# Optimization experiments

Hardware: AMD Instinct MI355X
Metric: run time of the kernel (lower is better)

## Reference

```python
import jax, jax.numpy as jnp
import numpy as np
from jax import lax

USER_NUM = 60000
ITEM_NUM = 40000
N_NODES = USER_NUM + ITEM_NUM
EMB = 64
NNZ = 3200000
N_LAYERS = 3
ALPHA = 0.1


def setup_inputs() -> dict:
    key = jax.random.key(0)
    k1, k2, k3, k4, k5 = jax.random.split(key, 5)
    rows = jax.random.randint(k1, (NNZ,), 0, N_NODES, dtype=jnp.int32)
    cols = jax.random.randint(k2, (NNZ,), 0, N_NODES, dtype=jnp.int32)
    # normalized adjacency values are small positives
    vals = jax.random.uniform(k3, (NNZ,), dtype=jnp.float32) * 0.05
    user_emb = jax.random.normal(k4, (USER_NUM, EMB), dtype=jnp.float32) * 0.1
    item_emb = jax.random.normal(k5, (ITEM_NUM, EMB), dtype=jnp.float32) * 0.1
    return {"rows": rows, "cols": cols, "vals": vals,
            "user_emb": user_emb, "item_emb": item_emb}


def reference(rows, cols, vals, user_emb, item_emb):
    # ego = cat(user, item); e_out starts at zeros (first forward call).
    ego = jnp.concatenate([user_emb, item_emb], axis=0)  # [N, d]
    e0 = jnp.zeros_like(ego)

    def step(e, _):
        # torch.sparse.mm(A, e.clone().detach()) -> SpMM with stop_gradient,
        # matching the original's detach of the propagated state.
        gathered = vals[:, None] * lax.stop_gradient(e)[cols]  # [nnz, d]
        msg = jax.ops.segment_sum(gathered, rows, num_segments=N_NODES)
        e_new = (1.0 - ALPHA) * msg + ego
        return e_new, None

    e_out, _ = lax.scan(step, e0, None, length=N_LAYERS)
    return e_out[:USER_NUM], e_out[USER_NUM:]
```

## Files before the change

### kernel.cpp

```cpp
#include <hip/hip_runtime.h>
#include <hip/hip_fp16.h>


#define USER_NUM 60000
#define ITEM_NUM 40000
#define N_NODES  100000
#define EMB      64
#define NNZ      3200000
#define OMA      0.9f
#define BR       128
#define NB       782
#define TILE     4096
#define CAP      4608

typedef float f32x4 __attribute__((ext_vector_type(4)));

__global__ __launch_bounds__(256) void ego_to_half(const float* __restrict__ ue,
                                                   const float* __restrict__ ie,
                                                   __half* __restrict__ dst) {
    int t = blockIdx.x * 256 + threadIdx.x;
    const int total8 = N_NODES * EMB / 8;
    if (t >= total8) return;
    size_t f0 = (size_t)t * 8;
    const size_t usz = (size_t)USER_NUM * EMB;
    const float4* s4 = (f0 < usz) ? (const float4*)(ue + f0)
                                  : (const float4*)(ie + (f0 - usz));
    float4 x = s4[0], y = s4[1];
    union { float4 f4; __half2 h2[4]; } o;
    o.h2[0] = __floats2half2_rn(x.x, x.y);
    o.h2[1] = __floats2half2_rn(x.z, x.w);
    o.h2[2] = __floats2half2_rn(y.x, y.y);
    o.h2[3] = __floats2half2_rn(y.z, y.w);
    ((float4*)dst)[t] = o.f4;
}

__global__ __launch_bounds__(256) void bucket_hist(const int* __restrict__ rows,
                                                   int* __restrict__ bcount) {
    __shared__ int lh[4][NB];
    int t = threadIdx.x, w = t >> 6;
    for (int b = t; b < 4 * NB; b += 256) lh[b / NB][b % NB] = 0;
    __syncthreads();
    int e0 = blockIdx.x * TILE;
#pragma unroll
    for (int j = 0; j < 16; ++j) {
        int i = e0 + t + 256 * j;
        if (i < NNZ) atomicAdd(&lh[w][rows[i] >> 7], 1);
    }
    __syncthreads();
    for (int b = t; b < NB; b += 256) {
        int c = lh[0][b] + lh[1][b] + lh[2][b] + lh[3][b];
        if (c) atomicAdd(&bcount[b], c);
    }
}

__global__ __launch_bounds__(256) void bucket_scan(const int* __restrict__ bcount,
                                                   int* __restrict__ bbase,
                                                   int* __restrict__ bcursor,
                                                   int* __restrict__ row_start) {
    __shared__ int ps[256];
    int t = threadIdx.x;
    int b0 = t * 4;
    int s = 0;
#pragma unroll
    for (int q = 0; q < 4; ++q) { int i = b0 + q; if (i < NB) s += bcount[i]; }
    ps[t] = s;
    __syncthreads();
    for (int off = 1; off < 256; off <<= 1) {
        int v = (t >= off) ? ps[t - off] : 0;
        __syncthreads();
        ps[t] += v;
        __syncthreads();
    }
    int excl = t ? ps[t - 1] : 0;
#pragma unroll
    for (int q = 0; q < 4; ++q) {
        int i = b0 + q;
        if (i < NB) { bbase[i] = excl; bcursor[i] = excl; excl += bcount[i]; }
    }
    if (t == 255) { bbase[NB] = ps[255]; row_start[N_NODES] = ps[255]; }
}

__global__ __launch_bounds__(256) void bucket_scatter(const int* __restrict__ rows,
                                                      const int* __restrict__ cols,
                                                      const float* __restrict__ vals,
                                                      int* __restrict__ bcursor,
                                                      int2* __restrict__ ebuf) {
    __shared__ int bins[NB + 1];
    __shared__ int lcur[NB];
    __shared__ int wsum[4];
    __shared__ int2 stage[TILE];
    int t = threadIdx.x;
    int lane = t & 63, w = t >> 6;
    for (int b = t; b <= NB; b += 256) bins[b] = 0;
    __syncthreads();

    int e0 = blockIdx.x * TILE;
    int mybk[16], mypk[16];
    float myv[16];
#pragma unroll
    for (int j = 0; j < 16; ++j) {
        int i = e0 + t + 256 * j;
        mybk[j] = -1;
        if (i < NNZ) {
            int r = rows[i], c = cols[i];
            myv[j]  = vals[i] * OMA;
            mybk[j] = r >> 7;
            mypk[j] = c | ((r & 127) << 17);
            atomicAdd(&bins[mybk[j]], 1);
        }
    }
    __syncthreads();

    int b0 = t * 4;
    int r0 = (b0     < NB) ? bins[b0]     : 0;
    int r1 = (b0 + 1 < NB) ? bins[b0 + 1] : 0;
    int r2 = (b0 + 2 < NB) ? bins[b0 + 2] : 0;
    int r3 = (b0 + 3 < NB) ? bins[b0 + 3] : 0;
    int s = r0 + r1 + r2 + r3;
    int incl = s;
#pragma unroll
    for (int off = 1; off < 64; off <<= 1) {
        int v = __shfl_up(incl, off, 64);
        if (lane >= off) incl += v;
    }
    if (lane == 63) wsum[w] = incl;
    __syncthreads();
    int prefix = 0;
#pragma unroll
    for (int i = 0; i < 4; ++i) if (i < w) prefix += wsum[i];
    int excl = prefix + incl - s;
    if (b0     < NB) { bins[b0]     = excl; lcur[b0]     = excl; excl += r0; }
    if (b0 + 1 < NB) { bins[b0 + 1] = excl; lcur[b0 + 1] = excl; excl += r1; }
    if (b0 + 2 < NB) { bins[b0 + 2] = excl; lcur[b0 + 2] = excl; excl += r2; }
    if (b0 + 3 < NB) { bins[b0 + 3] = excl; lcur[b0 + 3] = excl; excl += r3; }
    if (t == 255) bins[NB] = prefix + incl;
    __syncthreads();

#pragma unroll
    for (int j = 0; j < 16; ++j) {
        if (mybk[j] >= 0) {
            int p = atomicAdd(&lcur[mybk[j]], 1);
            stage[p] = make_int2(mypk[j], __float_as_int(myv[j]));
        }
    }
    __syncthreads();

    for (int b = t; b < NB; b += 256) {
        int src = bins[b];
        int cnt = bins[b + 1] - src;
        if (cnt > 0) {
            int g = atomicAdd(&bcursor[b], cnt);
            for (int q = 0; q < cnt; ++q) ebuf[g + q] = stage[src + q];
        }
    }
}

__global__ __launch_bounds__(256) void row_sort(const int* __restrict__ bbase,
                                                int2* __restrict__ ebuf,
                                                int* __restrict__ row_start) {
    __shared__ int2 stage[CAP];
    __shared__ int lhist[BR], lofs[BR], lcur[BR];
    int bk = blockIdx.x, t = threadIdx.x;
    int s = bbase[bk], e = bbase[bk + 1];
    int cnt = min(e - s, CAP);

    if (t < BR) lhist[t] = 0;
    __syncthreads();
    for (int i = t; i < cnt; i += 256) {
        int2 v = ebuf[s + i];
        stage[i] = v;
        atomicAdd(&lhist[(v.x >> 17) & 127], 1);
    }
    __syncthreads();
    if (t < 64) {
        int h0 = lhist[2 * t], h1 = lhist[2 * t + 1];
        int pair = h0 + h1;
        int incl = pair;
#pragma unroll
        for (int off = 1; off < 64; off <<= 1) {
            int v = __shfl_up(incl, off, 64);
            if (t >= off) incl += v;
        }
        int base = incl - pair;
        lofs[2 * t]     = base;      lcur[2 * t]     = base;
        lofs[2 * t + 1] = base + h0; lcur[2 * t + 1] = base + h0;
    }
    __syncthreads();
    if (t < BR) {
        int r = (bk << 7) + t;
        if (r < N_NODES) row_start[r] = s + lofs[t];
    }
    for (int i = t; i < cnt; i += 256) {
        int2 v = stage[i];
        int p = atomicAdd(&lcur[(v.x >> 17) & 127], 1);
        ebuf[s + p] = v;
    }
}

template <bool OUT_HALF>
__global__ __launch_bounds__(256) void spmm_pull_h(const int* __restrict__ row_start,
                                                   const int2* __restrict__ colval,
                                                   const __half* __restrict__ src,
                                                   const float* __restrict__ ue,
                                                   const float* __restrict__ ie,
                                                   void* __restrict__ outb) {
    int tid = blockIdx.x * 256 + threadIdx.x;
    int r = tid >> 4;
    if (r >= N_NODES) return;
    int lane  = threadIdx.x & 15;
    int qbase = (threadIdx.x & 63) & ~15;

    const float* egop = (r < USER_NUM) ? (ue + (size_t)r * EMB)
                                       : (ie + (size_t)(r - USER_NUM) * EMB);
    float4 acc = ((const float4*)egop)[lane];
    const float2* srcv = (const float2*)src;
    int s = row_start[r], e = row_start[r + 1];

    int2 cv = (s + lane < e) ? colval[s + lane] : make_int2(0, 0);
    for (int k = s; k < e; k += 16) {
        int idxn = k + 16 + lane;
        int2 nv = (idxn < e) ? colval[idxn] : make_int2(0, 0);
#pragma unroll
        for (int j = 0; j < 16; ++j) {
            int   cj = __shfl(cv.x, qbase + j, 64) & 0x1FFFF;
            float vj = __int_as_float(__shfl(cv.y, qbase + j, 64));
            union { float2 f2; __half2 h2[2]; } u;
            u.f2 = srcv[(size_t)cj * 16 + lane];
            float2 a = __half22float2(u.h2[0]);
            float2 b = __half22float2(u.h2[1]);
            acc.x += vj * a.x; acc.y += vj * a.y;
            acc.z += vj * b.x; acc.w += vj * b.y;
        }
        cv = nv;
    }
    if (OUT_HALF) {
        union { float2 f2; __half2 h2[2]; } o;
        o.h2[0] = __floats2half2_rn(acc.x, acc.y);
        o.h2[1] = __floats2half2_rn(acc.z, acc.w);
        ((float2*)outb)[(size_t)r * 16 + lane] = o.f2;
    } else {
        f32x4 av = { acc.x, acc.y, acc.z, acc.w };
        __builtin_nontemporal_store(av, &((f32x4*)outb)[(size_t)r * 16 + lane]);
    }
}

extern "C" void kernel_launch(void* const* d_in, const int* in_sizes, int n_in,
                              void* d_out, int out_size, void* d_ws, size_t ws_size,
                              hipStream_t stream) {
    const int*   rows = (const int*)d_in[0];
    const int*   cols = (const int*)d_in[1];
    const float* vals = (const float*)d_in[2];
    const float* ue   = (const float*)d_in[3];
    const float* ie   = (const float*)d_in[4];
    float* out = (float*)d_out;

    char* ws = (char*)d_ws;
    __half* ego_h    = (__half*)ws;
    __half* e2h      = (__half*)(ws + 12800000);
    int2*   ebuf     = (int2*)(ws + 25600000);
    int*    row_start= (int*)(ws + 51200000);
    int*    bcount   = (int*)(ws + 51600256);
    int*    bbase    = (int*)(ws + 51603456);
    int*    bcursor  = (int*)(ws + 51606656);

    (void)hipMemsetAsync(bcount, 0, NB * sizeof(int), stream);

    const int convBlocks = (N_NODES * EMB / 8 + 255) / 256;
    ego_to_half<<<convBlocks, 256, 0, stream>>>(ue, ie, ego_h);

    const int tiles = (NNZ + TILE - 1) / TILE;
    bucket_hist<<<tiles, 256, 0, stream>>>(rows, bcount);
    bucket_scan<<<1, 256, 0, stream>>>(bcount, bbase, bcursor, row_start);
    bucket_scatter<<<tiles, 256, 0, stream>>>(rows, cols, vals, bcursor, ebuf);
    row_sort<<<NB, 256, 0, stream>>>(bbase, ebuf, row_start);

    const int spmmBlocks = (N_NODES * 16 + 255) / 256;
    spmm_pull_h<true ><<<spmmBlocks, 256, 0, stream>>>(row_start, ebuf, ego_h, ue, ie, e2h);
    spmm_pull_h<false><<<spmmBlocks, 256, 0, stream>>>(row_start, ebuf, e2h,   ue, ie, out);
}
```

Before: 308.1 us.

## Use fixed-capacity buckets, drop histogram/scan passes, fuse row sort with first SpMM

Replaces the counting histogram and prefix scan with fixed-capacity bucket slots (CAPB per bucket) initialized inside the conversion kernel, so the scatter can run without a prior pass over rows. The per-bucket row sort is fused with the first SpMM layer, which then reads edges from the just-sorted bucket, and the scatter write-out now spreads a tile's entries across all threads using a binary search instead of one thread per bucket. Row extents become start/end pairs because buckets are no longer contiguous. This removes two kernels, a memset and a launch, but relies on no bucket exceeding its fixed capacity (any overflow would silently drop edges), and the fused kernel runs only 782 blocks for the first SpMM.

```diff
diff --git a/kernel.cpp b/kernel.cpp
--- a/kernel.cpp
+++ b/kernel.cpp
@@ -11,14 +11,16 @@
 #define BR       128
 #define NB       782
 #define TILE     4096
-#define CAP      4608
+#define CAPB     4480
 
 typedef float f32x4 __attribute__((ext_vector_type(4)));
 
-__global__ __launch_bounds__(256) void ego_to_half(const float* __restrict__ ue,
-                                                   const float* __restrict__ ie,
-                                                   __half* __restrict__ dst) {
+__global__ __launch_bounds__(256) void conv_init(const float* __restrict__ ue,
+                                                 const float* __restrict__ ie,
+                                                 __half* __restrict__ dst,
+                                                 int* __restrict__ bcursor) {
     int t = blockIdx.x * 256 + threadIdx.x;
+    if (t < NB) bcursor[t] = t * CAPB;
     const int total8 = N_NODES * EMB / 8;
     if (t >= total8) return;
     size_t f0 = (size_t)t * 8;
@@ -34,52 +36,6 @@
     ((float4*)dst)[t] = o.f4;
 }
 
-__global__ __launch_bounds__(256) void bucket_hist(const int* __restrict__ rows,
-                                                   int* __restrict__ bcount) {
-    __shared__ int lh[4][NB];
-    int t = threadIdx.x, w = t >> 6;
-    for (int b = t; b < 4 * NB; b += 256) lh[b / NB][b % NB] = 0;
-    __syncthreads();
-    int e0 = blockIdx.x * TILE;
-#pragma unroll
-    for (int j = 0; j < 16; ++j) {
-        int i = e0 + t + 256 * j;
-        if (i < NNZ) atomicAdd(&lh[w][rows[i] >> 7], 1);
-    }
-    __syncthreads();
-    for (int b = t; b < NB; b += 256) {
-        int c = lh[0][b] + lh[1][b] + lh[2][b] + lh[3][b];
-        if (c) atomicAdd(&bcount[b], c);
-    }
-}
-
-__global__ __launch_bounds__(256) void bucket_scan(const int* __restrict__ bcount,
-                                                   int* __restrict__ bbase,
-                                                   int* __restrict__ bcursor,
-                                                   int* __restrict__ row_start) {
-    __shared__ int ps[256];
-    int t = threadIdx.x;
-    int b0 = t * 4;
-    int s = 0;
-#pragma unroll
-    for (int q = 0; q < 4; ++q) { int i = b0 + q; if (i < NB) s += bcount[i]; }
-    ps[t] = s;
-    __syncthreads();
-    for (int off = 1; off < 256; off <<= 1) {
-        int v = (t >= off) ? ps[t - off] : 0;
-        __syncthreads();
-        ps[t] += v;
-        __syncthreads();
-    }
-    int excl = t ? ps[t - 1] : 0;
-#pragma unroll
-    for (int q = 0; q < 4; ++q) {
-        int i = b0 + q;
-        if (i < NB) { bbase[i] = excl; bcursor[i] = excl; excl += bcount[i]; }
-    }
-    if (t == 255) { bbase[NB] = ps[255]; row_start[N_NODES] = ps[255]; }
-}
-
 __global__ __launch_bounds__(256) void bucket_scatter(const int* __restrict__ rows,
                                                       const int* __restrict__ cols,
                                                       const float* __restrict__ vals,
@@ -146,34 +102,47 @@
     __syncthreads();
 
     for (int b = t; b < NB; b += 256) {
-        int src = bins[b];
-        int cnt = bins[b + 1] - src;
-        if (cnt > 0) {
-            int g = atomicAdd(&bcursor[b], cnt);
-            for (int q = 0; q < cnt; ++q) ebuf[g + q] = stage[src + q];
-        }
-    }
-}
-
-__global__ __launch_bounds__(256) void row_sort(const int* __restrict__ bbase,
-                                                int2* __restrict__ ebuf,
-                                                int* __restrict__ row_start) {
-    __shared__ int2 stage[CAP];
-    __shared__ int lhist[BR], lofs[BR], lcur[BR];
+        int st = bins[b], en = bins[b + 1];
+        int cnt = en - st;
+        if (cnt > 0) lcur[b] = atomicAdd(&bcursor[b], cnt) - st;
+    }
+    __syncthreads();
+
+    int total = bins[NB];
+    for (int i = t; i < total; i += 256) {
+        int lo = 0, hi = NB;
+        while (hi - lo > 1) {
+            int mid = (lo + hi) >> 1;
+            if (bins[mid] <= i) lo = mid; else hi = mid;
+        }
+        ebuf[(size_t)(lcur[lo] + i)] = stage[i];
+    }
+}
+
+__global__ __launch_bounds__(256) void sort_spmm1(const int* __restrict__ bcursor,
+                                                  int2* __restrict__ ebuf,
+                                                  int* __restrict__ row_start,
+                                                  int* __restrict__ row_end,
+                                                  const __half* __restrict__ ego_h,
+                                                  const float* __restrict__ ue,
+                                                  const float* __restrict__ ie,
+                                                  __half* __restrict__ e2h) {
+    __shared__ int2 stage[CAPB];
+    __shared__ int rhist[BR], rofs[BR], rcur[BR];
     int bk = blockIdx.x, t = threadIdx.x;
-    int s = bbase[bk], e = bbase[bk + 1];
-    int cnt = min(e - s, CAP);
-
-    if (t < BR) lhist[t] = 0;
+    int s = bk * CAPB;
+    int cnt = min(bcursor[bk] - s, CAPB);
+
+    if (t < BR) rhist[t] = 0;
     __syncthreads();
     for (int i = t; i < cnt; i += 256) {
-        int2 v = ebuf[s + i];
+        int2 v = ebuf[(size_t)(s + i)];
         stage[i] = v;
-        atomicAdd(&lhist[(v.x >> 17) & 127], 1);
+        atomicAdd(&rhist[(v.x >> 17) & 127], 1);
     }
     __syncthreads();
     if (t < 64) {
-        int h0 = lhist[2 * t], h1 = lhist[2 * t + 1];
+        int h0 = rhist[2 * t], h1 = rhist[2 * t + 1];
         int pair = h0 + h1;
         int incl = pair;
 #pragma unroll
@@ -182,28 +151,69 @@
             if (t >= off) incl += v;
         }
         int base = incl - pair;
-        lofs[2 * t]     = base;      lcur[2 * t]     = base;
-        lofs[2 * t + 1] = base + h0; lcur[2 * t + 1] = base + h0;
+        rofs[2 * t]     = base;      rcur[2 * t]     = base;
+        rofs[2 * t + 1] = base + h0; rcur[2 * t + 1] = base + h0;
     }
     __syncthreads();
     if (t < BR) {
         int r = (bk << 7) + t;
-        if (r < N_NODES) row_start[r] = s + lofs[t];
+        if (r < N_NODES) {
+            row_start[r] = s + rofs[t];
+            row_end[r]   = s + rofs[t] + rhist[t];
+        }
     }
     for (int i = t; i < cnt; i += 256) {
         int2 v = stage[i];
-        int p = atomicAdd(&lcur[(v.x >> 17) & 127], 1);
-        ebuf[s + p] = v;
-    }
-}
-
-template <bool OUT_HALF>
-__global__ __launch_bounds__(256) void spmm_pull_h(const int* __restrict__ row_start,
-                                                   const int2* __restrict__ colval,
-                                                   const __half* __restrict__ src,
-                                                   const float* __restrict__ ue,
-                                                   const float* __restrict__ ie,
-                                                   void* __restrict__ outb) {
+        int p = atomicAdd(&rcur[(v.x >> 17) & 127], 1);
+        ebuf[(size_t)(s + p)] = v;
+    }
+    __syncthreads();
+
+    int lane  = t & 15;
+    int qbase = (t & 63) & ~15;
+    int g = t >> 4;
+    const float2* srcv = (const float2*)ego_h;
+#pragma unroll
+    for (int rr = 0; rr < 8; ++rr) {
+        int rl = (g << 3) | rr;
+        int r  = (bk << 7) + rl;
+        if (r >= N_NODES) break;
+        const float* egop = (r < USER_NUM) ? (ue + (size_t)r * EMB)
+                                           : (ie + (size_t)(r - USER_NUM) * EMB);
+        float4 acc = ((const float4*)egop)[lane];
+        int ss = s + rofs[rl];
+        int ee = ss + rhist[rl];
+        int2 cv = (ss + lane < ee) ? ebuf[(size_t)(ss + lane)] : make_int2(0, 0);
+        for (int k = ss; k < ee; k += 16) {
+            int idxn = k + 16 + lane;
+            int2 nv = (idxn < ee) ? ebuf[(size_t)idxn] : make_int2(0, 0);
+#pragma unroll
+            for (int j = 0; j < 16; ++j) {
+                int   cj = __shfl(cv.x, qbase + j, 64) & 0x1FFFF;
+                float vj = __int_as_float(__shfl(cv.y, qbase + j, 64));
+                union { float2 f2; __half2 h2[2]; } u;
+                u.f2 = srcv[(size_t)cj * 16 + lane];
+                float2 a = __half22float2(u.h2[0]);
+                float2 b = __half22float2(u.h2[1]);
+                acc.x += vj * a.x; acc.y += vj * a.y;
+                acc.z += vj * b.x; acc.w += vj * b.y;
+            }
+            cv = nv;
+        }
+        union { float2 f2; __half2 h2[2]; } o;
+        o.h2[0] = __floats2half2_rn(acc.x, acc.y);
+        o.h2[1] = __floats2half2_rn(acc.z, acc.w);
+        ((float2*)e2h)[(size_t)r * 16 + lane] = o.f2;
+    }
+}
+
+__global__ __launch_bounds__(256) void spmm2(const int* __restrict__ row_start,
+                                             const int* __restrict__ row_end,
+                                             const int2* __restrict__ colval,
+                                             const __half* __restrict__ src,
+                                             const float* __restrict__ ue,
+                                             const float* __restrict__ ie,
+                                             float* __restrict__ outb) {
     int tid = blockIdx.x * 256 + threadIdx.x;
     int r = tid >> 4;
     if (r >= N_NODES) return;
@@ -214,12 +224,12 @@
                                        : (ie + (size_t)(r - USER_NUM) * EMB);
     float4 acc = ((const float4*)egop)[lane];
     const float2* srcv = (const float2*)src;
-    int s = row_start[r], e = row_start[r + 1];
-
-    int2 cv = (s + lane < e) ? colval[s + lane] : make_int2(0, 0);
+    int s = row_start[r], e = row_end[r];
+
+    int2 cv = (s + lane < e) ? colval[(size_t)(s + lane)] : make_int2(0, 0);
     for (int k = s; k < e; k += 16) {
         int idxn = k + 16 + lane;
-        int2 nv = (idxn < e) ? colval[idxn] : make_int2(0, 0);
+        int2 nv = (idxn < e) ? colval[(size_t)idxn] : make_int2(0, 0);
 #pragma unroll
         for (int j = 0; j < 16; ++j) {
             int   cj = __shfl(cv.x, qbase + j, 64) & 0x1FFFF;
@@ -233,15 +243,8 @@
         }
         cv = nv;
     }
-    if (OUT_HALF) {
-        union { float2 f2; __half2 h2[2]; } o;
-        o.h2[0] = __floats2half2_rn(acc.x, acc.y);
-        o.h2[1] = __floats2half2_rn(acc.z, acc.w);
-        ((float2*)outb)[(size_t)r * 16 + lane] = o.f2;
-    } else {
-        f32x4 av = { acc.x, acc.y, acc.z, acc.w };
-        __builtin_nontemporal_store(av, &((f32x4*)outb)[(size_t)r * 16 + lane]);
-    }
+    f32x4 av = { acc.x, acc.y, acc.z, acc.w };
+    __builtin_nontemporal_store(av, &((f32x4*)outb)[(size_t)r * 16 + lane]);
 }
 
 extern "C" void kernel_launch(void* const* d_in, const int* in_sizes, int n_in,
@@ -258,23 +261,17 @@
     __half* ego_h    = (__half*)ws;
     __half* e2h      = (__half*)(ws + 12800000);
     int2*   ebuf     = (int2*)(ws + 25600000);
-    int*    row_start= (int*)(ws + 51200000);
-    int*    bcount   = (int*)(ws + 51600256);
-    int*    bbase    = (int*)(ws + 51603456);
-    int*    bcursor  = (int*)(ws + 51606656);
-
-    (void)hipMemsetAsync(bcount, 0, NB * sizeof(int), stream);
+    int*    row_s    = (int*)(ws + 53626880);
+    int*    row_e    = (int*)(ws + 54026880);
+    int*    bcursor  = (int*)(ws + 54426880);
 
     const int convBlocks = (N_NODES * EMB / 8 + 255) / 256;
-    ego_to_half<<<convBlocks, 256, 0, stream>>>(ue, ie, ego_h);
+    conv_init<<<convBlocks, 256, 0, stream>>>(ue, ie, ego_h, bcursor);
 
     const int tiles = (NNZ + TILE - 1) / TILE;
-    bucket_hist<<<tiles, 256, 0, stream>>>(rows, bcount);
-    bucket_scan<<<1, 256, 0, stream>>>(bcount, bbase, bcursor, row_start);
     bucket_scatter<<<tiles, 256, 0, stream>>>(rows, cols, vals, bcursor, ebuf);
-    row_sort<<<NB, 256, 0, stream>>>(bbase, ebuf, row_start);
+    sort_spmm1<<<NB, 256, 0, stream>>>(bcursor, ebuf, row_s, row_e, ego_h, ue, ie, e2h);
 
     const int spmmBlocks = (N_NODES * 16 + 255) / 256;
-    spmm_pull_h<true ><<<spmmBlocks, 256, 0, stream>>>(row_start, ebuf, ego_h, ue, ie, e2h);
-    spmm_pull_h<false><<<spmmBlocks, 256, 0, stream>>>(row_start, ebuf, e2h,   ue, ie, out);
-}
+    spmm2<<<spmmBlocks, 256, 0, stream>>>(row_s, row_e, ebuf, e2h, ue, ie, out);
+}
```

After: 284.0 us. 7.8% less time.
